# Optimization experiments

Hardware: AMD Instinct MI355X
Metric: run time of the kernel (lower is better)

## Reference

```python
import jax, jax.numpy as jnp
import numpy as np

NEG_INF = -1e6  # d2l masked_softmax mask value

def setup_inputs() -> dict:
    key = jax.random.key(0)
    ks = jax.random.split(key, 6)
    B, Lq, Lk, dq, dv, H = 8, 256, 512, 256, 256, 64
    return {
        "queries": jax.random.normal(ks[0], (B, Lq, dq), jnp.float32),
        "keys": jax.random.normal(ks[1], (B, Lk, dq), jnp.float32),
        "values": jax.random.normal(ks[2], (B, Lk, dv), jnp.float32),
        "valid_lens": jax.random.randint(ks[3], (B,), 0, Lk),
        "W_q": jax.random.normal(ks[4], (H, dq), jnp.float32) * (dq ** -0.5),
        "W_k": jax.random.normal(ks[5], (H, dq), jnp.float32) * (dq ** -0.5),
        "w_v": jax.random.normal(jax.random.fold_in(key, 7), (H,), jnp.float32) * (H ** -0.5),
    }

def reference(queries, keys, values, valid_lens, W_q, W_k, w_v):
    # Project: [B,Lq,H], [B,Lk,H]
    q = jnp.einsum('bqd,hd->bqh', queries, W_q)
    k = jnp.einsum('bkd,hd->bkh', keys, W_k)
    # Broadcast-add + tanh: [B,Lq,Lk,H]
    features = jnp.tanh(q[:, :, None, :] + k[:, None, :, :])
    # Scalar projection -> scores [B,Lq,Lk]
    scores = jnp.einsum('bqkh,h->bqk', features, w_v)
    # masked_softmax over last axis with per-batch valid_lens
    Lk = keys.shape[1]
    mask = jnp.arange(Lk)[None, None, :] < valid_lens[:, None, None]
    scores = jnp.where(mask, scores, NEG_INF)
    attn = jax.nn.softmax(scores, axis=-1)
    # dropout p=0 (inference) -> identity; bmm with values
    return jnp.einsum('bqk,bkv->bqv', attn, values)
```

## Files before the change

### kernel.cpp

```cpp
#include <hip/hip_runtime.h>
#include <hip/hip_bf16.h>
#include <hip/hip_fp16.h>
#include <stdint.h>

#define NB 8
#define LQ 256
#define LK 512
#define NH 64
#define SCALE 2.8853900817779268f
#define L2E 1.4426950408889634f

#define QP_OFF   0
#define KP_OFF   131072
#define VBF_OFF  393216
#define PML_OFF  917504

extern "C" __device__ float __ocml_exp2_f32(float);
static __device__ __forceinline__ float fexp2(float x) {
#if __has_builtin(__builtin_amdgcn_exp2f)
  return __builtin_amdgcn_exp2f(x);
#else
  return __ocml_exp2_f32(x);
#endif
}
static __device__ __forceinline__ float frcp(float x) {
  return __builtin_amdgcn_rcpf(x);
}
static __device__ __forceinline__ uint16_t f2bf(float f) {
  uint32_t u = __float_as_uint(f);
  uint32_t r = (u + 0x7FFFu + ((u >> 16) & 1u)) >> 16;
  return (uint16_t)r;
}

typedef const __attribute__((address_space(1))) void* gas_ptr;
typedef __attribute__((address_space(3))) void* las_ptr;
static __device__ __forceinline__ void gload16(const void* g, void* l) {
  __builtin_amdgcn_global_load_lds((gas_ptr)g, (las_ptr)l, 16, 0, 0);
}

__global__ __launch_bounds__(256) void proj_kernel(
    const float* __restrict__ queries, const float* __restrict__ keys,
    const float* __restrict__ values,
    const float* __restrict__ Wq, const float* __restrict__ Wk,
    float* __restrict__ qp, float* __restrict__ kp, uint16_t* __restrict__ vbf)
{
  __shared__ float Wt[256][34];
  const int blk = blockIdx.x;
  const int t = threadIdx.x;

  if (blk >= 768) {
    int base = (blk - 768) * 16384 + t * 4;
#pragma unroll
    for (int it = 0; it < 16; ++it) {
      int idx = base + it * 1024;
      float4 v = *(const float4*)(values + idx);
      uint32_t lo = (uint32_t)f2bf(v.x) | ((uint32_t)f2bf(v.y) << 16);
      uint32_t hi = (uint32_t)f2bf(v.z) | ((uint32_t)f2bf(v.w) << 16);
      uint2 pk = {lo, hi};
      *(uint2*)(vbf + idx) = pk;
    }
    return;
  }

  const bool isQ = (blk < 256);
  const int sub = isQ ? blk : (blk - 256);
  const int tile = sub >> 1;
  const int hh = (sub & 1) * 32;
  const int rowbase = tile * 16;
  const float* __restrict__ X = isQ ? queries : keys;
  const float* __restrict__ W = isQ ? Wq : Wk;
  float* __restrict__ P = isQ ? qp : kp;

#pragma unroll 4
  for (int it = 0; it < 32; ++it) {
    Wt[t][it] = W[(hh + it) * 256 + t];
  }
  __syncthreads();

  const int ty = t >> 4;
  const int tx = t & 15;
  float a0 = 0.f, a1 = 0.f;

  const float* xr0 = X + (rowbase + ty) * 256;

#pragma unroll 4
  for (int d4 = 0; d4 < 64; ++d4) {
    int d = d4 * 4;
    float4 x0 = *(const float4*)(xr0 + d);
    float2 w0 = *(float2*)&Wt[d + 0][tx * 2];
    float2 w1 = *(float2*)&Wt[d + 1][tx * 2];
    float2 w2 = *(float2*)&Wt[d + 2][tx * 2];
    float2 w3 = *(float2*)&Wt[d + 3][tx * 2];
    a0 = fmaf(x0.x, w0.x, a0); a1 = fmaf(x0.x, w0.y, a1);
    a0 = fmaf(x0.y, w1.x, a0); a1 = fmaf(x0.y, w1.y, a1);
    a0 = fmaf(x0.z, w2.x, a0); a1 = fmaf(x0.z, w2.y, a1);
    a0 = fmaf(x0.w, w3.x, a0); a1 = fmaf(x0.w, w3.y, a1);
  }

  {
    int row = rowbase + ty;
    int h = hh + tx * 2;
    P[row * 64 + h + 0] = a0 * SCALE;
    P[row * 64 + h + 1] = a1 * SCALE;
  }
}

__global__ __launch_bounds__(256) void attn_kernel(
    const float* __restrict__ qp, const float* __restrict__ kp,
    const uint16_t* __restrict__ vbf, const float* __restrict__ w_v,
    const int* __restrict__ valid_lens, float* __restrict__ out,
    float* __restrict__ pml, __half* __restrict__ pacc, int nsplit)
{
  __shared__ float kTs[2][32][64];
  __shared__ uint16_t Vs[2][32][256];
  __shared__ float p_s[4][2][32];

  const int t = threadIdx.x;
  const int lane = t & 63;
  const int w = t >> 6;
  const int r2 = lane >> 5;
  const int kj = lane & 31;
  const int wg = blockIdx.x;
  const int b = wg & 7;
  const int qg = (wg >> 3) & 31;
  const int kh = wg >> 8;
  const int row = b * LQ + qg * 8 + w * 2 + r2;

  const int vl = valid_lens[b];
  const int n = (vl > 0) ? vl : LK;
  const int span = LK / nsplit;
  const int kstart = kh * span;
  int cnt = n - kstart;
  if (cnt > span) cnt = span;
  const int ntiles = (cnt > 0) ? ((cnt + 31) >> 5) : 0;

  if (ntiles == 0) {
    if (kj == 0) {
      pml[(row * nsplit + kh) * 2 + 0] = -1e30f;
      pml[(row * nsplit + kh) * 2 + 1] = 0.f;
    }
    return;
  }

  float W1 = 0.f;
#pragma unroll
  for (int g = 0; g < 16; ++g) {
    float4 wf = *(const float4*)(w_v + g * 4);
    W1 += (wf.x + wf.y) + (wf.z + wf.w);
  }

  float qv[64];
  {
    const float* qrow = qp + (size_t)row * 64;
#pragma unroll
    for (int i = 0; i < 16; ++i) {
      float4 v = *(const float4*)(qrow + i * 4);
      qv[i * 4 + 0] = v.x; qv[i * 4 + 1] = v.y;
      qv[i * 4 + 2] = v.z; qv[i * 4 + 3] = v.w;
    }
  }

  const float* kpb = kp + (size_t)(b * LK) * 64;
  const char* vbc = (const char*)(vbf + (size_t)b * LK * 256);

#define STAGE(BUF, K0) do { \
    int i0 = w * 2; \
    int kjr0 = i0 * 4 + (lane >> 4); \
    int cph = lane & 15; \
    gload16(kpb + (size_t)((K0) + kjr0) * 64 + (cph ^ (kjr0 & 7)) * 4, \
            &kTs[BUF][i0 * 4][0]); \
    int kjr1 = kjr0 + 4; \
    gload16(kpb + (size_t)((K0) + kjr1) * 64 + (cph ^ (kjr1 & 7)) * 4, \
            &kTs[BUF][i0 * 4 + 4][0]); \
    const char* vsrc = vbc + (size_t)(K0) * 512 + (size_t)w * 4096 + lane * 16; \
    gload16(vsrc + 0 * 1024, &Vs[BUF][w * 8 + 0][0]); \
    gload16(vsrc + 1 * 1024, &Vs[BUF][w * 8 + 2][0]); \
    gload16(vsrc + 2 * 1024, &Vs[BUF][w * 8 + 4][0]); \
    gload16(vsrc + 3 * 1024, &Vs[BUF][w * 8 + 6][0]); \
  } while (0)

  float m = -1e30f, l = 0.f;
  float acc[16];
#pragma unroll
  for (int i = 0; i < 16; ++i) acc[i] = 0.f;

  STAGE(0, kstart);

  for (int tt = 0; tt < ntiles; ++tt) {
    const int cur = tt & 1;
    const int k0 = kstart + tt * 32;
    if (tt + 1 < ntiles) {
      STAGE(cur ^ 1, k0 + 32);
      asm volatile("s_waitcnt vmcnt(6)" ::: "memory");
    } else {
      asm volatile("s_waitcnt vmcnt(0)" ::: "memory");
    }
    __builtin_amdgcn_sched_barrier(0);
    __builtin_amdgcn_s_barrier();
    __builtin_amdgcn_sched_barrier(0);
    __builtin_amdgcn_s_setprio(1);

    float r0 = 0.f, r1 = 0.f, r2a = 0.f, r3 = 0.f;
#pragma unroll
    for (int g = 0; g < 16; ++g) {
      float4 kf = *(const float4*)&kTs[cur][kj][((g ^ (kj & 7)) << 2)];
      float4 wf = *(const float4*)(w_v + g * 4);
      r0  = fmaf(wf.x, frcp(1.f + fexp2(qv[g * 4 + 0] + kf.x)), r0);
      r1  = fmaf(wf.y, frcp(1.f + fexp2(qv[g * 4 + 1] + kf.y)), r1);
      r2a = fmaf(wf.z, frcp(1.f + fexp2(qv[g * 4 + 2] + kf.z)), r2a);
      r3  = fmaf(wf.w, frcp(1.f + fexp2(qv[g * 4 + 3] + kf.w)), r3);
    }
    float racc = (r0 + r1) + (r2a + r3);

    float score;
    int kg = k0 + kj;
    if (vl == 0)      score = 0.f;
    else if (kg < n)  score = fmaf(-2.f, racc, W1);
    else              score = -1e30f;

    float mt = score;
#pragma unroll
    for (int s = 16; s; s >>= 1) mt = fmaxf(mt, __shfl_xor(mt, s, 64));
    float mnew = fmaxf(m, mt);
    float alpha = fexp2((m - mnew) * L2E);
    float p = fexp2((score - mnew) * L2E);
    m = mnew;
    float S = p;
#pragma unroll
    for (int s = 16; s; s >>= 1) S += __shfl_xor(S, s, 64);
    l = l * alpha + S;
    p_s[w][r2][kj] = p;

    float alpha_x = __shfl_xor(alpha, 32, 64);
    float a0 = (r2 == 0) ? alpha : alpha_x;
    float a1 = (r2 == 0) ? alpha_x : alpha;
#pragma unroll
    for (int i = 0; i < 8; ++i)  acc[i] *= a0;
#pragma unroll
    for (int i = 8; i < 16; ++i) acc[i] *= a1;

    const int c = kj;
#pragma unroll
    for (int i4 = 0; i4 < 4; ++i4) {
      float4 p0 = *(const float4*)&p_s[w][0][r2 * 16 + i4 * 4];
      float4 p1 = *(const float4*)&p_s[w][1][r2 * 16 + i4 * 4];
#pragma unroll
      for (int jj = 0; jj < 4; ++jj) {
        int kk = r2 * 16 + i4 * 4 + jj;
        uint4 vv = *(const uint4*)&Vs[cur][kk][c * 8];
        float pj0 = (jj == 0) ? p0.x : (jj == 1) ? p0.y : (jj == 2) ? p0.z : p0.w;
        float pj1 = (jj == 0) ? p1.x : (jj == 1) ? p1.y : (jj == 2) ? p1.z : p1.w;
        float f0 = __uint_as_float(vv.x << 16);
        float f1 = __uint_as_float(vv.x & 0xFFFF0000u);
        float f2 = __uint_as_float(vv.y << 16);
        float f3 = __uint_as_float(vv.y & 0xFFFF0000u);
        float f4 = __uint_as_float(vv.z << 16);
        float f5 = __uint_as_float(vv.z & 0xFFFF0000u);
        float f6 = __uint_as_float(vv.w << 16);
        float f7 = __uint_as_float(vv.w & 0xFFFF0000u);
        acc[0] = fmaf(pj0, f0, acc[0]);   acc[8]  = fmaf(pj1, f0, acc[8]);
        acc[1] = fmaf(pj0, f1, acc[1]);   acc[9]  = fmaf(pj1, f1, acc[9]);
        acc[2] = fmaf(pj0, f2, acc[2]);   acc[10] = fmaf(pj1, f2, acc[10]);
        acc[3] = fmaf(pj0, f3, acc[3]);   acc[11] = fmaf(pj1, f3, acc[11]);
        acc[4] = fmaf(pj0, f4, acc[4]);   acc[12] = fmaf(pj1, f4, acc[12]);
        acc[5] = fmaf(pj0, f5, acc[5]);   acc[13] = fmaf(pj1, f5, acc[13]);
        acc[6] = fmaf(pj0, f6, acc[6]);   acc[14] = fmaf(pj1, f6, acc[14]);
        acc[7] = fmaf(pj0, f7, acc[7]);   acc[15] = fmaf(pj1, f7, acc[15]);
      }
    }
    __builtin_amdgcn_s_setprio(0);
    __builtin_amdgcn_sched_barrier(0);
    __builtin_amdgcn_s_barrier();
  }
#undef STAGE

#pragma unroll
  for (int i = 0; i < 16; ++i) acc[i] += __shfl_xor(acc[i], 32, 64);

  const float* accr = acc + r2 * 8;
  if (nsplit == 1) {
    float inv = 1.f / l;
    float4 o0 = {accr[0] * inv, accr[1] * inv, accr[2] * inv, accr[3] * inv};
    float4 o1 = {accr[4] * inv, accr[5] * inv, accr[6] * inv, accr[7] * inv};
    float* op = out + (size_t)row * 256 + kj * 8;
    *(float4*)(op + 0) = o0;
    *(float4*)(op + 4) = o1;
  } else {
    if (kj == 0) {
      pml[(row * nsplit + kh) * 2 + 0] = m;
      pml[(row * nsplit + kh) * 2 + 1] = l;
    }
    __half2 h0 = __floats2half2_rn(accr[0], accr[1]);
    __half2 h1 = __floats2half2_rn(accr[2], accr[3]);
    __half2 h2 = __floats2half2_rn(accr[4], accr[5]);
    __half2 h3 = __floats2half2_rn(accr[6], accr[7]);
    uint4 pk = {*(uint32_t*)&h0, *(uint32_t*)&h1, *(uint32_t*)&h2, *(uint32_t*)&h3};
    *(uint4*)(pacc + ((size_t)(row * nsplit + kh)) * 256 + kj * 8) = pk;
  }
}

__global__ __launch_bounds__(256) void merge_kernel(
    const float* __restrict__ pml, const __half* __restrict__ pacc,
    float* __restrict__ out, int nsplit)
{
  const int t = threadIdx.x;
  const int row = blockIdx.x * 8 + (t >> 5);
  const int d8 = t & 31;

  float ms = -1e30f;
  for (int kh = 0; kh < nsplit; ++kh)
    ms = fmaxf(ms, pml[(row * nsplit + kh) * 2]);

  float L = 0.f;
  float o[8];
#pragma unroll
  for (int i = 0; i < 8; ++i) o[i] = 0.f;

  for (int kh = 0; kh < nsplit; ++kh) {
    float mk = pml[(row * nsplit + kh) * 2 + 0];
    float lk = pml[(row * nsplit + kh) * 2 + 1];
    if (lk > 0.f) {
      float e = fexp2((mk - ms) * L2E);
      L += e * lk;
      uint4 pk = *(const uint4*)(pacc + ((size_t)(row * nsplit + kh)) * 256 + d8 * 8);
      __half2 h0 = *(__half2*)&pk.x, h1 = *(__half2*)&pk.y;
      __half2 h2 = *(__half2*)&pk.z, h3 = *(__half2*)&pk.w;
      float2 f0 = __half22float2(h0), f1 = __half22float2(h1);
      float2 f2 = __half22float2(h2), f3 = __half22float2(h3);
      o[0] = fmaf(e, f0.x, o[0]); o[1] = fmaf(e, f0.y, o[1]);
      o[2] = fmaf(e, f1.x, o[2]); o[3] = fmaf(e, f1.y, o[3]);
      o[4] = fmaf(e, f2.x, o[4]); o[5] = fmaf(e, f2.y, o[5]);
      o[6] = fmaf(e, f3.x, o[6]); o[7] = fmaf(e, f3.y, o[7]);
    }
  }
  float inv = 1.f / L;
  float4 o0 = {o[0] * inv, o[1] * inv, o[2] * inv, o[3] * inv};
  float4 o1 = {o[4] * inv, o[5] * inv, o[6] * inv, o[7] * inv};
  float* op = out + (size_t)row * 256 + d8 * 8;
  *(float4*)(op + 0) = o0;
  *(float4*)(op + 4) = o1;
}

extern "C" void kernel_launch(void* const* d_in, const int* in_sizes, int n_in,
                              void* d_out, int out_size, void* d_ws, size_t ws_size,
                              hipStream_t stream) {
  const float* queries    = (const float*)d_in[0];
  const float* keys       = (const float*)d_in[1];
  const float* values     = (const float*)d_in[2];
  const int*   valid_lens = (const int*)d_in[3];
  const float* Wq         = (const float*)d_in[4];
  const float* Wk         = (const float*)d_in[5];
  const float* w_v        = (const float*)d_in[6];
  float* out = (float*)d_out;

  float* ws = (float*)d_ws;
  float* qp  = ws + QP_OFF;
  float* kp  = ws + KP_OFF;
  uint16_t* vbf = (uint16_t*)(ws + VBF_OFF);
  float* pml = ws + PML_OFF;

  int nsplit;
  if      (ws_size >= (size_t)PML_OFF * 4 + 2048u * 4 * 8 + 2048u * 4 * 512) nsplit = 4;
  else if (ws_size >= (size_t)PML_OFF * 4 + 2048u * 2 * 8 + 2048u * 2 * 512) nsplit = 2;
  else nsplit = 1;
  __half* pacc = (__half*)(pml + (size_t)2048 * nsplit * 2);

  hipLaunchKernelGGL(proj_kernel, dim3(832), dim3(256), 0, stream,
                     queries, keys, values, Wq, Wk, qp, kp, vbf);
  hipLaunchKernelGGL(attn_kernel, dim3(nsplit * 256), dim3(256), 0, stream,
                     qp, kp, vbf, w_v, valid_lens, out, pml, pacc, nsplit);
  if (nsplit > 1) {
    hipLaunchKernelGGL(merge_kernel, dim3(256), dim3(256), 0, stream,
                       pml, pacc, out, nsplit);
  }
}
```

Measured before the change: 44.97 us.

## Drop online-softmax max tracking using bounded scores; stage projection inputs in LDS

Scores are bounded because tanh lies in [-1,1], so the attention kernel drops the running max, rescaling and shuffle reductions and computes exp directly from a fused FMA. The split partials become plain fp32 sums, which lets the merge kernel just add them, and empty splits now write zeros. The projection kernel also stages its 16 input rows in shared memory before the dot-product loop. This writes twice as much partial data as the fp16 version and relies on the score bound to avoid exp overflow.

After: 45.26 us. About the same (+0.7%).

```diff
diff --git a/kernel.cpp b/kernel.cpp
--- a/kernel.cpp
+++ b/kernel.cpp
@@ -13,7 +13,7 @@
 #define QP_OFF   0
 #define KP_OFF   131072
 #define VBF_OFF  393216
-#define PML_OFF  917504
+#define PL_OFF   917504
 
 extern "C" __device__ float __ocml_exp2_f32(float);
 static __device__ __forceinline__ float fexp2(float x) {
@@ -45,6 +45,7 @@
     float* __restrict__ qp, float* __restrict__ kp, uint16_t* __restrict__ vbf)
 {
   __shared__ float Wt[256][34];
+  __shared__ float Xs[16][260];
   const int blk = blockIdx.x;
   const int t = threadIdx.x;
 
@@ -75,18 +76,23 @@
   for (int it = 0; it < 32; ++it) {
     Wt[t][it] = W[(hh + it) * 256 + t];
   }
+#pragma unroll
+  for (int i = 0; i < 4; ++i) {
+    int flat4 = t + i * 256;
+    int r = flat4 >> 6, d4 = flat4 & 63;
+    float4 v = *(const float4*)(X + (size_t)(rowbase + r) * 256 + d4 * 4);
+    *(float4*)&Xs[r][d4 * 4] = v;
+  }
   __syncthreads();
 
   const int ty = t >> 4;
   const int tx = t & 15;
   float a0 = 0.f, a1 = 0.f;
 
-  const float* xr0 = X + (rowbase + ty) * 256;
-
 #pragma unroll 4
   for (int d4 = 0; d4 < 64; ++d4) {
     int d = d4 * 4;
-    float4 x0 = *(const float4*)(xr0 + d);
+    float4 x0 = *(const float4*)&Xs[ty][d];
     float2 w0 = *(float2*)&Wt[d + 0][tx * 2];
     float2 w1 = *(float2*)&Wt[d + 1][tx * 2];
     float2 w2 = *(float2*)&Wt[d + 2][tx * 2];
@@ -109,7 +115,7 @@
     const float* __restrict__ qp, const float* __restrict__ kp,
     const uint16_t* __restrict__ vbf, const float* __restrict__ w_v,
     const int* __restrict__ valid_lens, float* __restrict__ out,
-    float* __restrict__ pml, __half* __restrict__ pacc, int nsplit)
+    float* __restrict__ pl, float* __restrict__ pacc, int nsplit)
 {
   __shared__ float kTs[2][32][64];
   __shared__ uint16_t Vs[2][32][256];
@@ -119,7 +125,7 @@
   const int lane = t & 63;
   const int w = t >> 6;
   const int r2 = lane >> 5;
-  const int kj = lane & 31;
+  const int kx = lane & 31;
   const int wg = blockIdx.x;
   const int b = wg & 7;
   const int qg = (wg >> 3) & 31;
@@ -135,10 +141,11 @@
   const int ntiles = (cnt > 0) ? ((cnt + 31) >> 5) : 0;
 
   if (ntiles == 0) {
-    if (kj == 0) {
-      pml[(row * nsplit + kh) * 2 + 0] = -1e30f;
-      pml[(row * nsplit + kh) * 2 + 1] = 0.f;
-    }
+    if (kx == 0) pl[row * nsplit + kh] = 0.f;
+    float4 z = {0.f, 0.f, 0.f, 0.f};
+    float* pa = pacc + ((size_t)(row * nsplit + kh)) * 256 + kx * 8;
+    *(float4*)(pa + 0) = z;
+    *(float4*)(pa + 4) = z;
     return;
   }
 
@@ -148,6 +155,7 @@
     float4 wf = *(const float4*)(w_v + g * 4);
     W1 += (wf.x + wf.y) + (wf.z + wf.w);
   }
+  const float W1L = W1 * L2E;
 
   float qv[64];
   {
@@ -179,7 +187,7 @@
     gload16(vsrc + 3 * 1024, &Vs[BUF][w * 8 + 6][0]); \
   } while (0)
 
-  float m = -1e30f, l = 0.f;
+  float l = 0.f;
   float acc[16];
 #pragma unroll
   for (int i = 0; i < 16; ++i) acc[i] = 0.f;
@@ -203,7 +211,7 @@
     float r0 = 0.f, r1 = 0.f, r2a = 0.f, r3 = 0.f;
 #pragma unroll
     for (int g = 0; g < 16; ++g) {
-      float4 kf = *(const float4*)&kTs[cur][kj][((g ^ (kj & 7)) << 2)];
+      float4 kf = *(const float4*)&kTs[cur][kx][((g ^ (kx & 7)) << 2)];
       float4 wf = *(const float4*)(w_v + g * 4);
       r0  = fmaf(wf.x, frcp(1.f + fexp2(qv[g * 4 + 0] + kf.x)), r0);
       r1  = fmaf(wf.y, frcp(1.f + fexp2(qv[g * 4 + 1] + kf.y)), r1);
@@ -212,34 +220,17 @@
     }
     float racc = (r0 + r1) + (r2a + r3);
 
-    float score;
-    int kg = k0 + kj;
-    if (vl == 0)      score = 0.f;
-    else if (kg < n)  score = fmaf(-2.f, racc, W1);
-    else              score = -1e30f;
-
-    float mt = score;
-#pragma unroll
-    for (int s = 16; s; s >>= 1) mt = fmaxf(mt, __shfl_xor(mt, s, 64));
-    float mnew = fmaxf(m, mt);
-    float alpha = fexp2((m - mnew) * L2E);
-    float p = fexp2((score - mnew) * L2E);
-    m = mnew;
-    float S = p;
-#pragma unroll
-    for (int s = 16; s; s >>= 1) S += __shfl_xor(S, s, 64);
-    l = l * alpha + S;
-    p_s[w][r2][kj] = p;
-
-    float alpha_x = __shfl_xor(alpha, 32, 64);
-    float a0 = (r2 == 0) ? alpha : alpha_x;
-    float a1 = (r2 == 0) ? alpha_x : alpha;
-#pragma unroll
-    for (int i = 0; i < 8; ++i)  acc[i] *= a0;
-#pragma unroll
-    for (int i = 8; i < 16; ++i) acc[i] *= a1;
-
-    const int c = kj;
+    float pe = fexp2(fmaf(-SCALE, racc, W1L));
+    int kg = k0 + kx;
+    float p;
+    if (vl == 0)      p = 1.f;
+    else if (kg < n)  p = pe;
+    else              p = 0.f;
+
+    l += p;
+    p_s[w][r2][kx] = p;
+
+    const int c = kx;
 #pragma unroll
     for (int i4 = 0; i4 < 4; ++i4) {
       float4 p0 = *(const float4*)&p_s[w][0][r2 * 16 + i4 * 4];
@@ -276,62 +267,47 @@
 
 #pragma unroll
   for (int i = 0; i < 16; ++i) acc[i] += __shfl_xor(acc[i], 32, 64);
+#pragma unroll
+  for (int s = 16; s; s >>= 1) l += __shfl_xor(l, s, 64);
 
   const float* accr = acc + r2 * 8;
   if (nsplit == 1) {
     float inv = 1.f / l;
     float4 o0 = {accr[0] * inv, accr[1] * inv, accr[2] * inv, accr[3] * inv};
     float4 o1 = {accr[4] * inv, accr[5] * inv, accr[6] * inv, accr[7] * inv};
-    float* op = out + (size_t)row * 256 + kj * 8;
+    float* op = out + (size_t)row * 256 + kx * 8;
     *(float4*)(op + 0) = o0;
     *(float4*)(op + 4) = o1;
   } else {
-    if (kj == 0) {
-      pml[(row * nsplit + kh) * 2 + 0] = m;
-      pml[(row * nsplit + kh) * 2 + 1] = l;
-    }
-    __half2 h0 = __floats2half2_rn(accr[0], accr[1]);
-    __half2 h1 = __floats2half2_rn(accr[2], accr[3]);
-    __half2 h2 = __floats2half2_rn(accr[4], accr[5]);
-    __half2 h3 = __floats2half2_rn(accr[6], accr[7]);
-    uint4 pk = {*(uint32_t*)&h0, *(uint32_t*)&h1, *(uint32_t*)&h2, *(uint32_t*)&h3};
-    *(uint4*)(pacc + ((size_t)(row * nsplit + kh)) * 256 + kj * 8) = pk;
+    if (kx == 0) pl[row * nsplit + kh] = l;
+    float* pa = pacc + ((size_t)(row * nsplit + kh)) * 256 + kx * 8;
+    float4 a0 = {accr[0], accr[1], accr[2], accr[3]};
+    float4 a1 = {accr[4], accr[5], accr[6], accr[7]};
+    *(float4*)(pa + 0) = a0;
+    *(float4*)(pa + 4) = a1;
   }
 }
 
 __global__ __launch_bounds__(256) void merge_kernel(
-    const float* __restrict__ pml, const __half* __restrict__ pacc,
+    const float* __restrict__ pl, const float* __restrict__ pacc,
     float* __restrict__ out, int nsplit)
 {
   const int t = threadIdx.x;
   const int row = blockIdx.x * 8 + (t >> 5);
   const int d8 = t & 31;
 
-  float ms = -1e30f;
-  for (int kh = 0; kh < nsplit; ++kh)
-    ms = fmaxf(ms, pml[(row * nsplit + kh) * 2]);
-
   float L = 0.f;
   float o[8];
 #pragma unroll
   for (int i = 0; i < 8; ++i) o[i] = 0.f;
 
   for (int kh = 0; kh < nsplit; ++kh) {
-    float mk = pml[(row * nsplit + kh) * 2 + 0];
-    float lk = pml[(row * nsplit + kh) * 2 + 1];
-    if (lk > 0.f) {
-      float e = fexp2((mk - ms) * L2E);
-      L += e * lk;
-      uint4 pk = *(const uint4*)(pacc + ((size_t)(row * nsplit + kh)) * 256 + d8 * 8);
-      __half2 h0 = *(__half2*)&pk.x, h1 = *(__half2*)&pk.y;
-      __half2 h2 = *(__half2*)&pk.z, h3 = *(__half2*)&pk.w;
-      float2 f0 = __half22float2(h0), f1 = __half22float2(h1);
-      float2 f2 = __half22float2(h2), f3 = __half22float2(h3);
-      o[0] = fmaf(e, f0.x, o[0]); o[1] = fmaf(e, f0.y, o[1]);
-      o[2] = fmaf(e, f1.x, o[2]); o[3] = fmaf(e, f1.y, o[3]);
-      o[4] = fmaf(e, f2.x, o[4]); o[5] = fmaf(e, f2.y, o[5]);
-      o[6] = fmaf(e, f3.x, o[6]); o[7] = fmaf(e, f3.y, o[7]);
-    }
+    L += pl[row * nsplit + kh];
+    const float* pa = pacc + ((size_t)(row * nsplit + kh)) * 256 + d8 * 8;
+    float4 a0 = *(const float4*)(pa + 0);
+    float4 a1 = *(const float4*)(pa + 4);
+    o[0] += a0.x; o[1] += a0.y; o[2] += a0.z; o[3] += a0.w;
+    o[4] += a1.x; o[5] += a1.y; o[6] += a1.z; o[7] += a1.w;
   }
   float inv = 1.f / L;
   float4 o0 = {o[0] * inv, o[1] * inv, o[2] * inv, o[3] * inv};
@@ -357,20 +333,20 @@
   float* qp  = ws + QP_OFF;
   float* kp  = ws + KP_OFF;
   uint16_t* vbf = (uint16_t*)(ws + VBF_OFF);
-  float* pml = ws + PML_OFF;
+  float* pl  = ws + PL_OFF;
 
   int nsplit;
-  if      (ws_size >= (size_t)PML_OFF * 4 + 2048u * 4 * 8 + 2048u * 4 * 512) nsplit = 4;
-  else if (ws_size >= (size_t)PML_OFF * 4 + 2048u * 2 * 8 + 2048u * 2 * 512) nsplit = 2;
+  if      (ws_size >= (size_t)PL_OFF * 4 + 2048u * 4 * 4 + 2048u * 4 * 1024) nsplit = 4;
+  else if (ws_size >= (size_t)PL_OFF * 4 + 2048u * 2 * 4 + 2048u * 2 * 1024) nsplit = 2;
   else nsplit = 1;
-  __half* pacc = (__half*)(pml + (size_t)2048 * nsplit * 2);
+  float* pacc = pl + (size_t)2048 * nsplit;
 
   hipLaunchKernelGGL(proj_kernel, dim3(832), dim3(256), 0, stream,
                      queries, keys, values, Wq, Wk, qp, kp, vbf);
   hipLaunchKernelGGL(attn_kernel, dim3(nsplit * 256), dim3(256), 0, stream,
-                     qp, kp, vbf, w_v, valid_lens, out, pml, pacc, nsplit);
+                     qp, kp, vbf, w_v, valid_lens, out, pl, pacc, nsplit);
   if (nsplit > 1) {
     hipLaunchKernelGGL(merge_kernel, dim3(256), dim3(256), 0, stream,
-                       pml, pacc, out, nsplit);
-  }
-}
+                       pl, pacc, out, nsplit);
+  }
+}
```
